# Optimization experiments

Hardware: AMD Instinct MI355X
Metric: run time of the kernel (lower is better)

The kernel has to match this reference:

```python
import jax, jax.numpy as jnp
import numpy as np

NUM_TREES = 32
TREE_DEPTH = 6
INPUT_DIM = 256
SHRINKAGE = 0.1
PHI_NUMEL = 1
N_INTERNAL = (1 << TREE_DEPTH) - 1  # 63, heap-ordered (level by level)
N_LEAVES = 1 << TREE_DEPTH          # 64


def setup_inputs() -> dict:
    key = jax.random.key(0)
    kx, kw, kb, kp = jax.random.split(key, 4)
    x = jax.random.normal(kx, (16384, INPUT_DIM), dtype=jnp.float32)
    # All internal-node Linear(input_dim,1) weights, batched: [T, N, F], biases [T, N]
    lim = 1.0 / np.sqrt(INPUT_DIM)  # torch nn.Linear default uniform init scale
    W = jax.random.uniform(kw, (NUM_TREES, N_INTERNAL, INPUT_DIM), minval=-lim, maxval=lim, dtype=jnp.float32)
    b = jax.random.uniform(kb, (NUM_TREES, N_INTERNAL), minval=-lim, maxval=lim, dtype=jnp.float32)
    # Leaf values phi: [T, L, P] (original: randn per leaf)
    phi = jax.random.normal(kp, (NUM_TREES, N_LEAVES, PHI_NUMEL), dtype=jnp.float32)
    return {"x": x, "W": W, "b": b, "phi": phi}


def reference(x, W, b, phi):
    B = x.shape[0]
    T, N, F = W.shape
    # One batched GEMM for every internal node of every tree, then sigmoid.
    # probs[b, t, n] = sigmoid(x[b] . W[t, n] + b[t, n]); heap order: node n at
    # level d occupies slots [2^d - 1, 2^(d+1) - 2], children of slot i are 2i, 2i+1.
    probs = jax.nn.sigmoid(jnp.einsum('bf,tnf->btn', x, W) + b)  # [B, T, N]
    # Path probabilities down the tree: left child gets (1 - p), right gets p
    # (matches calculate_probabilities: left <- pp*(1-prob), right <- pp*prob).
    mu = jnp.ones((B, T, 1), dtype=probs.dtype)
    offset = 0
    depth = int(np.log2(N + 1))
    for d in range(depth):
        n = 1 << d
        p = probs[:, :, offset:offset + n]                      # [B, T, n]
        mu = jnp.stack([mu * (1.0 - p), mu * p], axis=-1)       # [B, T, n, 2]
        mu = mu.reshape(B, T, 2 * n)
        offset += n
    # mu: [B, T, L] leaf path probabilities. Per-tree pred = sum_l mu_l * phi_l;
    # GBM output = shrinkage * sum over trees.
    pred = SHRINKAGE * jnp.einsum('btl,tlp->bp', mu, phi)       # [B, P]
    return pred
```

## Files before the change

### kernel.cpp

```cpp
#include <hip/hip_runtime.h>
#include <cmath>

typedef unsigned short u16;
typedef __bf16 bf16x8 __attribute__((ext_vector_type(8)));
typedef float f32x4 __attribute__((ext_vector_type(4)));
typedef unsigned short u16x4 __attribute__((ext_vector_type(4)));

#define BATCH 16384
#define NTREE 32
#define NINT 63
#define NLEAF 64
#define FDIM 256
#define MT 128

typedef __attribute__((address_space(3))) void lvoid;
typedef __attribute__((address_space(1))) const void gvoid;
__device__ __forceinline__ void gload16(const void* g, void* l) {
    __builtin_amdgcn_global_load_lds((gvoid*)g, (lvoid*)l, 16, 0, 0);
}

__device__ __forceinline__ u16 f2bf(float f) {
    unsigned int x = __float_as_uint(f);
    x += 0x7fffu + ((x >> 16) & 1u);
    return (u16)(x >> 16);
}

__device__ __forceinline__ int slot2node(int slot) {
    int lg = (slot >> 2) & 3;
    int v = ((slot >> 4) << 2) | (slot & 3);
    if (v == 0)  return (lg & 1) ? (1 + (lg >> 1)) : 0;
    if (v == 1)  return 3 + lg;
    if (v < 4)   return 7 + 2 * lg + (v - 2);
    if (v < 8)   return 15 + 4 * lg + (v - 4);
    return 31 + 8 * lg + (v - 8);
}

__global__ void convert_kernel(const float* __restrict__ x, const float* __restrict__ W,
                               const float* __restrict__ b,
                               u16* __restrict__ xb, u16* __restrict__ Wb,
                               float* __restrict__ bperm) {
    int idx = blockIdx.x * blockDim.x + threadIdx.x;
    int stride = gridDim.x * blockDim.x;
    const int NXQ = BATCH * FDIM / 4;
    for (int i = idx; i < NXQ; i += stride) {
        float4 v = ((const float4*)x)[i];
        u16x4 o = { f2bf(v.x), f2bf(v.y), f2bf(v.z), f2bf(v.w) };
        ((u16x4*)xb)[i] = o;
    }
    const int NWQ = NTREE * NLEAF * FDIM / 4;
    for (int i = idx; i < NWQ; i += stride) {
        int t = i / (NLEAF * FDIM / 4);
        int r = i % (NLEAF * FDIM / 4);
        int slot = r / (FDIM / 4);
        int kq = r % (FDIM / 4);
        int node = slot2node(slot);
        float4 v = ((const float4*)(W + ((size_t)t * NINT + node) * FDIM))[kq];
        u16x4 o = { f2bf(v.x), f2bf(v.y), f2bf(v.z), f2bf(v.w) };
        ((u16x4*)Wb)[i] = o;
    }
    if (idx < NTREE * NLEAF)
        bperm[idx] = b[(idx >> 6) * NINT + slot2node(idx & 63)];
}

__global__ __launch_bounds__(256, 2) void softgbm_main(
    const u16* __restrict__ xb, const u16* __restrict__ Wb,
    const float* __restrict__ bperm, const float* __restrict__ phig,
    float* __restrict__ partial) {
    __shared__ u16 X[MT * FDIM];

    const int tid = threadIdx.x;
    const int lane = tid & 63, wv = tid >> 6;
    const int t = blockIdx.y * 4 + wv;
    const int m0 = blockIdx.x * MT;
    const int frow = lane & 15, lg = lane >> 4, f7 = frow & 7;

    #pragma unroll
    for (int i = 0; i < 16; ++i) {
        int cl = i * 256 + tid;
        int row = cl >> 5, pcc = cl & 31;
        int cc = (pcc & 24) | ((pcc & 7) ^ (row & 7));
        gload16(xb + (size_t)(m0 + row) * FDIM + cc * 8, &X[cl * 8]);
    }

    const u16* wbase = Wb + (size_t)t * NLEAF * FDIM + frow * FDIM + lg * 8;
    bf16x8 wfr[4][8];
    #pragma unroll
    for (int ar = 0; ar < 4; ++ar)
        #pragma unroll
        for (int ks = 0; ks < 8; ++ks)
            wfr[ar][ks] = *(const bf16x8*)(wbase + ar * 16 * FDIM + ks * 32);

    int xoff[8];
    #pragma unroll
    for (int ks = 0; ks < 8; ++ks) {
        int cx = ks * 4 + lg;
        xoff[ks] = ((cx & 24) | ((cx & 7) ^ f7)) * 16;
    }

    __syncthreads();

    #pragma unroll
    for (int half = 0; half < 2; ++half) {
        f32x4 acc[4][4];
        #pragma unroll
        for (int ar = 0; ar < 4; ++ar)
            #pragma unroll
            for (int j = 0; j < 4; ++j) {
                float bv = bperm[t * 64 + ar * 16 + lg * 4 + j];
                #pragma unroll
                for (int bc = 0; bc < 4; ++bc) acc[ar][bc][j] = bv;
            }

        const char* Xc = (const char*)X;
        int rbase[4];
        #pragma unroll
        for (int bc = 0; bc < 4; ++bc)
            rbase[bc] = (half * 64 + bc * 16 + frow) * 512;

        #pragma unroll
        for (int ks = 0; ks < 8; ++ks) {
            bf16x8 xf[4];
            #pragma unroll
            for (int bc = 0; bc < 4; ++bc)
                xf[bc] = *(const bf16x8*)(Xc + rbase[bc] + xoff[ks]);
            #pragma unroll
            for (int ar = 0; ar < 4; ++ar)
                #pragma unroll
                for (int bc = 0; bc < 4; ++bc)
                    acc[ar][bc] = __builtin_amdgcn_mfma_f32_16x16x32_bf16(wfr[ar][ks], xf[bc], acc[ar][bc], 0, 0, 0);
        }

        float pha[8], phd[8];
        #pragma unroll
        for (int i = 0; i < 8; ++i) {
            float2 p2 = *(const float2*)&phig[(size_t)t * NLEAF + lg * 16 + 2 * i];
            pha[i] = p2.x; phd[i] = p2.y - p2.x;
        }
        float tot[4];
        #pragma unroll
        for (int bc = 0; bc < 4; ++bc) {
            float pv[16];
            #pragma unroll
            for (int v2 = 0; v2 < 16; ++v2)
                pv[v2] = __builtin_amdgcn_rcpf(1.f + __expf(-acc[v2 >> 2][bc][v2 & 3]));
            float o = __shfl_xor(pv[0], 16);
            float proot = (lg & 1) ? o : pv[0];
            float pd1   = (lg & 1) ? pv[0] : o;
            float mb = ((lg >> 1) ? proot : 1.f - proot) * ((lg & 1) ? pd1 : 1.f - pd1);
            float m3[2], m4[4], m5[8];
            { float t1 = mb * pv[1]; m3[1] = t1; m3[0] = mb - t1; }
            #pragma unroll
            for (int i = 0; i < 2; ++i) { float t1 = m3[i] * pv[2 + i]; m4[2*i+1] = t1; m4[2*i] = m3[i] - t1; }
            #pragma unroll
            for (int i = 0; i < 4; ++i) { float t1 = m4[i] * pv[4 + i]; m5[2*i+1] = t1; m5[2*i] = m4[i] - t1; }
            float s = 0.f;
            #pragma unroll
            for (int i = 0; i < 8; ++i) s += m5[i] * (pha[i] + pv[8 + i] * phd[i]);
            s += __shfl_xor(s, 16);
            s += __shfl_xor(s, 32);
            tot[bc] = s;
        }
        float vout = (lg & 2) ? ((lg & 1) ? tot[3] : tot[2])
                              : ((lg & 1) ? tot[1] : tot[0]);
        partial[(size_t)t * BATCH + m0 + half * 64 + lane] = vout;
    }
}

__global__ void reduce_kernel(const float* __restrict__ partial, float* __restrict__ out) {
    int i = blockIdx.x * 256 + threadIdx.x;
    float s = 0.f;
    #pragma unroll
    for (int t = 0; t < NTREE; ++t) s += partial[(size_t)t * BATCH + i];
    out[i] = 0.1f * s;
}

extern "C" void kernel_launch(void* const* d_in, const int* in_sizes, int n_in,
                              void* d_out, int out_size, void* d_ws, size_t ws_size,
                              hipStream_t stream) {
    const float* x   = (const float*)d_in[0];
    const float* W   = (const float*)d_in[1];
    const float* b   = (const float*)d_in[2];
    const float* phi = (const float*)d_in[3];
    float* out = (float*)d_out;

    u16* xb = (u16*)d_ws;
    u16* Wb = xb + (size_t)BATCH * FDIM;
    float* partial = (float*)(Wb + (size_t)NTREE * NLEAF * FDIM);
    float* bperm = partial + (size_t)NTREE * BATCH;

    convert_kernel<<<2048, 256, 0, stream>>>(x, W, b, xb, Wb, bperm);
    softgbm_main<<<dim3(BATCH / MT, NTREE / 4), 256, 0, stream>>>(xb, Wb, bperm, phi, partial);
    reduce_kernel<<<BATCH / 256, 256, 0, stream>>>(partial, out);
}
```

Measured before the change: 43.74 us.

## Restructure main GEMM into double-buffered K-loop with both operands staged in LDS

```diff
diff --git a/kernel.cpp b/kernel.cpp
--- a/kernel.cpp
+++ b/kernel.cpp
@@ -12,6 +12,9 @@
 #define NLEAF 64
 #define FDIM 256
 #define MT 128
+#define TPB 2
+#define BK 64
+#define KSTEPS 4
 
 typedef __attribute__((address_space(3))) void lvoid;
 typedef __attribute__((address_space(1))) const void gvoid;
@@ -66,104 +69,123 @@
     const u16* __restrict__ xb, const u16* __restrict__ Wb,
     const float* __restrict__ bperm, const float* __restrict__ phig,
     float* __restrict__ partial) {
-    __shared__ u16 X[MT * FDIM];
+    __shared__ u16 Ash[2][MT * BK];
+    __shared__ u16 Bsh[2][MT * BK];
 
     const int tid = threadIdx.x;
     const int lane = tid & 63, wv = tid >> 6;
-    const int t = blockIdx.y * 4 + wv;
+    const int t0 = blockIdx.y * TPB;
     const int m0 = blockIdx.x * MT;
+    const int tp = wv & 1, rg = wv >> 1;
     const int frow = lane & 15, lg = lane >> 4, f7 = frow & 7;
-
-    #pragma unroll
-    for (int i = 0; i < 16; ++i) {
-        int cl = i * 256 + tid;
-        int row = cl >> 5, pcc = cl & 31;
-        int cc = (pcc & 24) | ((pcc & 7) ^ (row & 7));
-        gload16(xb + (size_t)(m0 + row) * FDIM + cc * 8, &X[cl * 8]);
-    }
-
-    const u16* wbase = Wb + (size_t)t * NLEAF * FDIM + frow * FDIM + lg * 8;
-    bf16x8 wfr[4][8];
+    const int t = t0 + tp;
+
+    const u16* agp[4]; const u16* bgp[4]; int ldst[4];
+    #pragma unroll
+    for (int j = 0; j < 4; ++j) {
+        int cl = j * 256 + tid;
+        int row = cl >> 3, pcc = cl & 7;
+        int cc = pcc ^ (row & 7);
+        agp[j] = Wb + (size_t)(t0 * NLEAF + row) * FDIM + cc * 8;
+        bgp[j] = xb + (size_t)(m0 + row) * FDIM + cc * 8;
+        ldst[j] = cl * 8;
+    }
+
+    int aoffs[4][2], boffs[4][2];
+    #pragma unroll
+    for (int ar = 0; ar < 4; ++ar) {
+        int r = tp * 64 + ar * 16 + frow;
+        #pragma unroll
+        for (int ks = 0; ks < 2; ++ks) {
+            int cc = ks * 4 + lg;
+            aoffs[ar][ks] = r * 128 + ((cc ^ (r & 7)) * 16);
+        }
+    }
+    #pragma unroll
+    for (int bc = 0; bc < 4; ++bc) {
+        int n = rg * 64 + bc * 16 + frow;
+        #pragma unroll
+        for (int ks = 0; ks < 2; ++ks) {
+            int cc = ks * 4 + lg;
+            boffs[bc][ks] = n * 128 + ((cc ^ (n & 7)) * 16);
+        }
+    }
+
+    #pragma unroll
+    for (int j = 0; j < 4; ++j) {
+        gload16(agp[j], &Ash[0][ldst[j]]);
+        gload16(bgp[j], &Bsh[0][ldst[j]]);
+    }
+    float pha[8], phd[8];
+    #pragma unroll
+    for (int i = 0; i < 8; ++i) {
+        float2 p2 = *(const float2*)&phig[(size_t)t * NLEAF + lg * 16 + 2 * i];
+        pha[i] = p2.x; phd[i] = p2.y - p2.x;
+    }
+    f32x4 acc[4][4];
     #pragma unroll
     for (int ar = 0; ar < 4; ++ar)
         #pragma unroll
-        for (int ks = 0; ks < 8; ++ks)
-            wfr[ar][ks] = *(const bf16x8*)(wbase + ar * 16 * FDIM + ks * 32);
-
-    int xoff[8];
-    #pragma unroll
-    for (int ks = 0; ks < 8; ++ks) {
-        int cx = ks * 4 + lg;
-        xoff[ks] = ((cx & 24) | ((cx & 7) ^ f7)) * 16;
-    }
-
-    __syncthreads();
-
-    #pragma unroll
-    for (int half = 0; half < 2; ++half) {
-        f32x4 acc[4][4];
-        #pragma unroll
-        for (int ar = 0; ar < 4; ++ar)
+        for (int j = 0; j < 4; ++j) {
+            float bv = bperm[t * 64 + ar * 16 + lg * 4 + j];
+            #pragma unroll
+            for (int bc = 0; bc < 4; ++bc) acc[ar][bc][j] = bv;
+        }
+
+    #pragma unroll
+    for (int st = 0; st < KSTEPS; ++st) {
+        __syncthreads();
+        if (st < KSTEPS - 1) {
             #pragma unroll
             for (int j = 0; j < 4; ++j) {
-                float bv = bperm[t * 64 + ar * 16 + lg * 4 + j];
-                #pragma unroll
-                for (int bc = 0; bc < 4; ++bc) acc[ar][bc][j] = bv;
+                gload16(agp[j] + (st + 1) * BK, &Ash[(st + 1) & 1][ldst[j]]);
+                gload16(bgp[j] + (st + 1) * BK, &Bsh[(st + 1) & 1][ldst[j]]);
             }
-
-        const char* Xc = (const char*)X;
-        int rbase[4];
-        #pragma unroll
-        for (int bc = 0; bc < 4; ++bc)
-            rbase[bc] = (half * 64 + bc * 16 + frow) * 512;
-
-        #pragma unroll
-        for (int ks = 0; ks < 8; ++ks) {
-            bf16x8 xf[4];
-            #pragma unroll
-            for (int bc = 0; bc < 4; ++bc)
-                xf[bc] = *(const bf16x8*)(Xc + rbase[bc] + xoff[ks]);
+        }
+        const char* Ab = (const char*)Ash[st & 1];
+        const char* Bb = (const char*)Bsh[st & 1];
+        #pragma unroll
+        for (int ks = 0; ks < 2; ++ks) {
+            bf16x8 af[4], bf_[4];
+            #pragma unroll
+            for (int ar = 0; ar < 4; ++ar) af[ar] = *(const bf16x8*)(Ab + aoffs[ar][ks]);
+            #pragma unroll
+            for (int bc = 0; bc < 4; ++bc) bf_[bc] = *(const bf16x8*)(Bb + boffs[bc][ks]);
             #pragma unroll
             for (int ar = 0; ar < 4; ++ar)
                 #pragma unroll
                 for (int bc = 0; bc < 4; ++bc)
-                    acc[ar][bc] = __builtin_amdgcn_mfma_f32_16x16x32_bf16(wfr[ar][ks], xf[bc], acc[ar][bc], 0, 0, 0);
-        }
-
-        float pha[8], phd[8];
-        #pragma unroll
-        for (int i = 0; i < 8; ++i) {
-            float2 p2 = *(const float2*)&phig[(size_t)t * NLEAF + lg * 16 + 2 * i];
-            pha[i] = p2.x; phd[i] = p2.y - p2.x;
-        }
-        float tot[4];
-        #pragma unroll
-        for (int bc = 0; bc < 4; ++bc) {
-            float pv[16];
-            #pragma unroll
-            for (int v2 = 0; v2 < 16; ++v2)
-                pv[v2] = __builtin_amdgcn_rcpf(1.f + __expf(-acc[v2 >> 2][bc][v2 & 3]));
-            float o = __shfl_xor(pv[0], 16);
-            float proot = (lg & 1) ? o : pv[0];
-            float pd1   = (lg & 1) ? pv[0] : o;
-            float mb = ((lg >> 1) ? proot : 1.f - proot) * ((lg & 1) ? pd1 : 1.f - pd1);
-            float m3[2], m4[4], m5[8];
-            { float t1 = mb * pv[1]; m3[1] = t1; m3[0] = mb - t1; }
-            #pragma unroll
-            for (int i = 0; i < 2; ++i) { float t1 = m3[i] * pv[2 + i]; m4[2*i+1] = t1; m4[2*i] = m3[i] - t1; }
-            #pragma unroll
-            for (int i = 0; i < 4; ++i) { float t1 = m4[i] * pv[4 + i]; m5[2*i+1] = t1; m5[2*i] = m4[i] - t1; }
-            float s = 0.f;
-            #pragma unroll
-            for (int i = 0; i < 8; ++i) s += m5[i] * (pha[i] + pv[8 + i] * phd[i]);
-            s += __shfl_xor(s, 16);
-            s += __shfl_xor(s, 32);
-            tot[bc] = s;
-        }
-        float vout = (lg & 2) ? ((lg & 1) ? tot[3] : tot[2])
-                              : ((lg & 1) ? tot[1] : tot[0]);
-        partial[(size_t)t * BATCH + m0 + half * 64 + lane] = vout;
-    }
+                    acc[ar][bc] = __builtin_amdgcn_mfma_f32_16x16x32_bf16(af[ar], bf_[bc], acc[ar][bc], 0, 0, 0);
+        }
+    }
+
+    float tot[4];
+    #pragma unroll
+    for (int bc = 0; bc < 4; ++bc) {
+        float pv[16];
+        #pragma unroll
+        for (int v2 = 0; v2 < 16; ++v2)
+            pv[v2] = __builtin_amdgcn_rcpf(1.f + __expf(-acc[v2 >> 2][bc][v2 & 3]));
+        float o = __shfl_xor(pv[0], 16);
+        float proot = (lg & 1) ? o : pv[0];
+        float pd1   = (lg & 1) ? pv[0] : o;
+        float mb = ((lg >> 1) ? proot : 1.f - proot) * ((lg & 1) ? pd1 : 1.f - pd1);
+        float m3[2], m4[4], m5[8];
+        { float t1 = mb * pv[1]; m3[1] = t1; m3[0] = mb - t1; }
+        #pragma unroll
+        for (int i = 0; i < 2; ++i) { float t1 = m3[i] * pv[2 + i]; m4[2*i+1] = t1; m4[2*i] = m3[i] - t1; }
+        #pragma unroll
+        for (int i = 0; i < 4; ++i) { float t1 = m4[i] * pv[4 + i]; m5[2*i+1] = t1; m5[2*i] = m4[i] - t1; }
+        float s = 0.f;
+        #pragma unroll
+        for (int i = 0; i < 8; ++i) s += m5[i] * (pha[i] + pv[8 + i] * phd[i]);
+        s += __shfl_xor(s, 16);
+        s += __shfl_xor(s, 32);
+        tot[bc] = s;
+    }
+    float vout = (lg & 2) ? ((lg & 1) ? tot[3] : tot[2])
+                          : ((lg & 1) ? tot[1] : tot[0]);
+    partial[(size_t)t * BATCH + m0 + rg * 64 + lane] = vout;
 }
 
 __global__ void reduce_kernel(const float* __restrict__ partial, float* __restrict__ out) {
@@ -189,6 +211,6 @@
     float* bperm = partial + (size_t)NTREE * BATCH;
 
     convert_kernel<<<2048, 256, 0, stream>>>(x, W, b, xb, Wb, bperm);
-    softgbm_main<<<dim3(BATCH / MT, NTREE / 4), 256, 0, stream>>>(xb, Wb, bperm, phi, partial);
+    softgbm_main<<<dim3(BATCH / MT, NTREE / TPB), 256, 0, stream>>>(xb, Wb, bperm, phi, partial);
     reduce_kernel<<<BATCH / 256, 256, 0, stream>>>(partial, out);
 }
```

Result: faster. 40.43 us (-7.6%).
